# Optimization experiments

Hardware: AMD Instinct MI355X
Metric: run time of the kernel (lower is better)

The kernel has to match this reference:

```python
import jax, jax.numpy as jnp
import numpy as np

C, P, G = 80, 30000, 800       # classes, preds/class, gts/class
IOU_THR = 0.5
IMG = 1024.0                   # synthetic image size
BATCH = 16                     # images per batch (box[0] = image index)


def _make_boxes(key, n_cls, n):
    """Boxes in the module's 7-col layout: [img_idx, class, score, x1, y1, x2, y2]."""
    k1, k2, k3, k4 = jax.random.split(key, 4)
    xy = jax.random.uniform(k1, (n_cls, n, 2), minval=0.0, maxval=IMG - 128.0)
    wh = jax.random.uniform(k2, (n_cls, n, 2), minval=4.0, maxval=128.0)
    score = jax.random.uniform(k3, (n_cls, n, 1))
    img_idx = jax.random.randint(k4, (n_cls, n, 1), 0, BATCH).astype(jnp.float32)
    cls = jnp.zeros((n_cls, n, 1), jnp.float32)
    return jnp.concatenate([img_idx, cls, score, xy, xy + wh], axis=-1)


def setup_inputs() -> dict:
    key = jax.random.key(0)
    kp, kg = jax.random.split(key)
    return {"pred_boxes": _make_boxes(kp, C, P), "gt_boxes": _make_boxes(kg, C, G)}


def _pairwise_iou(a, b):
    # a: [P,4], b: [G,4] corner-format xyxy -> [P,G]
    lt = jnp.maximum(a[:, None, :2], b[None, :, :2])
    rb = jnp.minimum(a[:, None, 2:], b[None, :, 2:])
    wh = jnp.clip(rb - lt, 0.0)
    inter = wh[..., 0] * wh[..., 1]
    area_a = (a[:, 2] - a[:, 0]) * (a[:, 3] - a[:, 1])
    area_b = (b[:, 2] - b[:, 0]) * (b[:, 3] - b[:, 1])
    return inter / (area_a[:, None] + area_b[None, :] - inter + 1e-9)


def _ap_one_class(pb, gb):
    # pb: [P,7] preds, gb: [G,7] gts for one class
    n_p, n_g = pb.shape[0], gb.shape[0]
    order = jnp.argsort(-pb[:, 2])             # sort preds by score desc
    boxes = pb[order, 3:7]
    iou = _pairwise_iou(boxes, gb[:, 3:7])     # [P,G]
    best_iou = iou.max(axis=1)
    match = iou.argmax(axis=1)                 # best gt per pred
    valid = best_iou > IOU_THR
    p_idx = jnp.arange(n_p, dtype=jnp.int32)
    # first (highest-score) valid pred claiming each gt -> TP; later claims -> FP
    first = jnp.full((n_g,), n_p, jnp.int32).at[match].min(
        jnp.where(valid, p_idx, n_p))
    tp = (valid & (p_idx == first[match])).astype(jnp.float32)
    ctp = jnp.cumsum(tp)
    cfp = jnp.cumsum(1.0 - tp)
    recall = ctp / (n_g + 1e-9)
    precision = ctp / (ctp + cfp + 1e-9)
    # trapezoidal AP over the PR curve (torch.trapz(precisions, recalls))
    return jnp.sum((recall[1:] - recall[:-1]) * (precision[1:] + precision[:-1]) * 0.5)


def reference(pred_boxes, gt_boxes):
    # sequential map over classes keeps peak memory at one [P,G] IoU matrix
    aps = jax.lax.map(lambda ab: _ap_one_class(ab[0], ab[1]), (pred_boxes, gt_boxes))
    return jnp.mean(aps)
```

## Files before the change

### kernel.cpp

```cpp
#include <hip/hip_runtime.h>

#define C 80
#define P 30000
#define G 800
#define BS 256
#define NB 16
#define NC (NB * NB)
#define PPTM 8
#define TPBM (BS * PPTM)
#define HCH 8
#define CHSZ ((P + HCH - 1) / HCH)


__device__ __forceinline__ unsigned long long pack_key(float s, int p) {
    return ((unsigned long long)__float_as_uint(s) << 32) | (unsigned)(P - 1 - p);
}

__device__ __forceinline__ int cell_coord(float v) {
    return min(max((int)(v * (1.0f / 64.0f)), 0), NB - 1);
}

__device__ __forceinline__ int cell_of_center(float cxf, float cyf) {
    return cell_coord(cyf) * NB + cell_coord(cxf);
}

__global__ __launch_bounds__(BS) void gt_bin_kernel(
        const float* __restrict__ gt,
        unsigned short* __restrict__ gtCnt, unsigned short* __restrict__ gtOff,
        float4* __restrict__ gtBox, float* __restrict__ gtAbe,
        unsigned short* __restrict__ gtIdx,
        unsigned long long* __restrict__ gtKey, int* __restrict__ gHist,
        int* __restrict__ predCnt, int* __restrict__ predCur,
        unsigned int* __restrict__ doneCnt) {
    __shared__ int h[NC], cur[NC];
    __shared__ int gcell[G];
    const int c = blockIdx.x, tid = threadIdx.x;
    h[tid] = 0;
    predCnt[c * NC + tid] = 0;
    predCur[c * NC + tid] = 0;
    if (c == 0 && tid == 0) *doneCnt = 0u;
    for (int i = tid; i < G; i += BS) gtKey[c * G + i] = 0ull;
    for (int j = tid; j < 1024; j += BS) gHist[c * 1024 + j] = 0;
    __syncthreads();
    for (int i = tid; i < G; i += BS) {
        const float* r = gt + ((size_t)c * G + i) * 7;
        int cl = cell_of_center(0.5f * (r[3] + r[5]), 0.5f * (r[4] + r[6]));
        gcell[i] = cl;
        atomicAdd(&h[cl], 1);
    }
    __syncthreads();
    const int v = h[tid];
    cur[tid] = v;
    __syncthreads();
    for (int o = 1; o < NC; o <<= 1) {
        int t = (tid >= o) ? cur[tid - o] : 0;
        __syncthreads();
        cur[tid] += t;
        __syncthreads();
    }
    const int excl = cur[tid] - v;
    gtOff[c * NC + tid] = (unsigned short)excl;
    gtCnt[c * NC + tid] = (unsigned short)v;
    __syncthreads();
    cur[tid] = excl;
    __syncthreads();
    for (int i = tid; i < G; i += BS) {
        const float* r = gt + ((size_t)c * G + i) * 7;
        float x1 = r[3], y1 = r[4], x2 = r[5], y2 = r[6];
        int slot = atomicAdd(&cur[gcell[i]], 1);
        gtBox[c * G + slot] = make_float4(x1, y1, x2, y2);
        gtAbe[c * G + slot] = __fadd_rn(__fmul_rn(__fsub_rn(x2, x1), __fsub_rn(y2, y1)), 1e-9f);
        gtIdx[c * G + slot] = (unsigned short)i;
    }
}

__global__ __launch_bounds__(BS) void pprep_kernel(
        const float* __restrict__ pred, int* __restrict__ predCnt,
        unsigned char* __restrict__ cellB) {
    __shared__ int h[NC];
    const int c = blockIdx.y, tid = threadIdx.x;
    h[tid] = 0;
    __syncthreads();
    int p = blockIdx.x * BS + tid;
    if (p < P) {
        const float* r = pred + ((size_t)c * P + p) * 7;
        int cl = cell_of_center(0.5f * (r[3] + r[5]), 0.5f * (r[4] + r[6]));
        cellB[(size_t)c * P + p] = (unsigned char)cl;
        atomicAdd(&h[cl], 1);
    }
    __syncthreads();
    if (h[tid]) atomicAdd(&predCnt[c * NC + tid], h[tid]);
}

__global__ __launch_bounds__(BS) void pscatter_kernel(
        const unsigned char* __restrict__ cellB, const int* __restrict__ predCnt,
        int* __restrict__ predCur, unsigned short* __restrict__ pIdxS) {
    __shared__ int h[NC], base[NC], sc[NC];
    const int c = blockIdx.y, tid = threadIdx.x;
    h[tid] = 0;
    sc[tid] = predCnt[c * NC + tid];
    const int v = sc[tid];
    __syncthreads();
    int p = blockIdx.x * BS + tid;
    int cellv = 0, lr = 0;
    if (p < P) {
        cellv = cellB[(size_t)c * P + p];
        lr = atomicAdd(&h[cellv], 1);
    }
    __syncthreads();
    for (int o = 1; o < NC; o <<= 1) {
        int t = (tid >= o) ? sc[tid - o] : 0;
        __syncthreads();
        sc[tid] += t;
        __syncthreads();
    }
    if (h[tid]) base[tid] = (sc[tid] - v) + atomicAdd(&predCur[c * NC + tid], h[tid]);
    __syncthreads();
    if (p < P) pIdxS[(size_t)c * P + base[cellv] + lr] = (unsigned short)p;
}

__global__ __launch_bounds__(BS) void match10_kernel(
        const float* __restrict__ pred, const unsigned short* __restrict__ pIdxS,
        const unsigned short* __restrict__ gtOff, const unsigned short* __restrict__ gtCnt,
        const float4* __restrict__ gtBox, const float* __restrict__ gtAbe,
        const unsigned short* __restrict__ gtIdx,
        unsigned long long* __restrict__ gtKey) {
    __shared__ float4 sB[G];
    __shared__ float  sE[G];
    __shared__ unsigned short sG[G];
    __shared__ unsigned short sOff[NC], sCnt[NC];
    const int c = blockIdx.y, tid = threadIdx.x;
    const int s0 = blockIdx.x * TPBM;

    for (int i = tid; i < G; i += BS) {
        sB[i] = gtBox[c * G + i];
        sE[i] = gtAbe[c * G + i];
        sG[i] = gtIdx[c * G + i];
    }
    sOff[tid] = gtOff[c * NC + tid];
    sCnt[tid] = gtCnt[c * NC + tid];
    __syncthreads();

    const size_t cp = (size_t)c * P;
    #pragma unroll 1
    for (int rep = 0; rep < PPTM; ++rep) {
        const int slot = s0 + rep * BS + tid;
        if (slot < P) {
            const int p = pIdxS[cp + slot];
            const float* r = pred + (cp + p) * 7;
            float ax1 = r[3], ay1 = r[4], ax2 = r[5], ay2 = r[6];
            float A = __fmul_rn(__fsub_rn(ax2, ax1), __fsub_rn(ay2, ay1));
            const int x0 = cell_coord(ax1), x1 = cell_coord(ax2);
            const int y0 = cell_coord(ay1), y1 = cell_coord(ay2);
            float IN = 0.0f, SB = 1.0f;
            int mj = -1;
            for (int yy = y0; yy <= y1; ++yy) {
                const int rowb = yy * NB;
                const int jb = sOff[rowb + x0];
                const int je = sOff[rowb + x1] + sCnt[rowb + x1];
                #pragma unroll 2
                for (int j = jb; j < je; ++j) {
                    float4 b = sB[j];
                    float lx = fmaxf(ax1, b.x), ly = fmaxf(ay1, b.y);
                    float rx = fminf(ax2, b.z), ry = fminf(ay2, b.w);
                    float wx = fmaxf(__fsub_rn(rx, lx), 0.0f);
                    float wy = fmaxf(__fsub_rn(ry, ly), 0.0f);
                    float in = __fmul_rn(wx, wy);
                    float sb = __fadd_rn(A, sE[j]);
                    bool  up = __fmul_rn(in, SB) > __fmul_rn(IN, sb);
                    IN = up ? in : IN; SB = up ? sb : SB; mj = up ? j : mj;
                }
            }
            if (IN > 0.0f) {
                float4 b = sB[mj];
                float area = __fmul_rn(__fsub_rn(b.z, b.x), __fsub_rn(b.w, b.y));
                float dn = __fadd_rn(__fsub_rn(__fadd_rn(A, area), IN), 1e-9f);
                float iou = __fdiv_rn(IN, dn);
                if (iou > 0.5f) {
                    float sscore = r[2];
                    atomicMax(&gtKey[c * G + sG[mj]], pack_key(sscore, p));
                }
            }
        }
    }
}

__global__ __launch_bounds__(BS) void histf_kernel(
        const float* __restrict__ pred,
        const unsigned long long* __restrict__ gtKey,
        int* __restrict__ gHist, int* __restrict__ sortT) {
    __shared__ unsigned long long k[G];
    __shared__ unsigned long long sk[1024];
    __shared__ int h[1024];
    __shared__ int cnt;
    const int c = blockIdx.y, chunk = blockIdx.x, tid = threadIdx.x;

    if (tid == 0) cnt = 0;
    for (int j = tid; j < 1024; j += BS) { sk[j] = 0ull; h[j] = 0; }
    __syncthreads();
    for (int i = tid; i < G; i += BS) {
        unsigned long long key = gtKey[c * G + i];
        if (key != 0ull) k[atomicAdd(&cnt, 1)] = key;
    }
    __syncthreads();
    const int T = cnt;
    if (chunk == 0 && tid == 0) sortT[c] = T;

    for (int t = tid; t < T; t += BS) {
        unsigned long long key = k[t];
        int pos = 0;
        for (int u = 0; u < T; ++u) pos += (k[u] > key) ? 1 : 0;
        sk[pos] = key;
    }
    __syncthreads();

    const int start = chunk * CHSZ;
    const int end   = min(start + CHSZ, P);
    const float* pr = pred + (size_t)c * P * 7;
    for (int i = start + tid; i < end; i += BS) {
        unsigned long long kq =
            ((unsigned long long)__float_as_uint(pr[(size_t)i * 7 + 2]) << 32)
            | (unsigned)(P - 1 - i);
        int lo = 0;
        #pragma unroll
        for (int step = 512; step > 0; step >>= 1)
            if (sk[lo + step - 1] > kq) lo += step;
        atomicAdd(&h[lo], 1);
    }
    __syncthreads();
    for (int j = tid; j < 1024; j += BS)
        if (h[j]) atomicAdd(&gHist[c * 1024 + j], h[j]);
}

__global__ __launch_bounds__(BS) void ap2m_kernel(
        const int* __restrict__ sortT, const int* __restrict__ gHist,
        float* __restrict__ ap, unsigned int* __restrict__ doneCnt,
        float* __restrict__ out) {
    __shared__ int ha[1024];
    __shared__ int hb[1024];
    __shared__ float red[BS];
    const int c = blockIdx.x, tid = threadIdx.x;
    const int T = sortT[c];
    for (int j = tid; j < 1024; j += BS) ha[j] = gHist[c * 1024 + j];
    __syncthreads();
    int* src = ha; int* dst = hb;
    for (int o = 1; o < 1024; o <<= 1) {
        for (int j = tid; j < 1024; j += BS)
            dst[j] = src[j] + ((j >= o) ? src[j - o] : 0);
        __syncthreads();
        int* tmp = src; src = dst; dst = tmp;
    }
    float sum = 0.0f;
    for (int s = tid; s < T; s += BS) {
        int r = src[s] - 1;
        if (r >= 1) {
            float kf  = (float)(s + 1);
            float km  = (float)s;
            float ri  = __fdiv_rn(kf, 800.0f);
            float rim = __fdiv_rn(km, 800.0f);
            float pi  = __fdiv_rn(kf, (float)(r + 1));
            float pim = __fdiv_rn(km, (float)r);
            sum = __fadd_rn(sum,
                  __fmul_rn(__fmul_rn(__fsub_rn(ri, rim), __fadd_rn(pi, pim)), 0.5f));
        }
    }
    red[tid] = sum;
    __syncthreads();
    for (int s2 = BS / 2; s2 > 0; s2 >>= 1) {
        if (tid < s2) red[tid] = __fadd_rn(red[tid], red[tid + s2]);
        __syncthreads();
    }
    if (tid == 0) {
        ap[c] = red[0];
        __threadfence();
        unsigned int t = atomicAdd(doneCnt, 1u);
        if (t == C - 1) {
            __threadfence();
            float s = 0.0f;
            for (int c2 = 0; c2 < C; ++c2) s = __fadd_rn(s, ap[c2]);
            out[0] = __fdiv_rn(s, 80.0f);
        }
    }
}

extern "C" void kernel_launch(void* const* d_in, const int* in_sizes, int n_in,
                              void* d_out, int out_size, void* d_ws, size_t ws_size,
                              hipStream_t stream) {
    const float* pred = (const float*)d_in[0];
    const float* gt   = (const float*)d_in[1];
    float* out = (float*)d_out;

    char* ws = (char*)d_ws;
    int*                sortT      = (int*)               (ws + 0);
    float*              ap         = (float*)             (ws + 512);
    unsigned int*       doneCnt    = (unsigned int*)      (ws + 896);
    int*                predCnt    = (int*)               (ws + 1024);
    int*                predCur    = (int*)               (ws + 82944);
    unsigned short*     gtCnt      = (unsigned short*)    (ws + 164864);
    unsigned short*     gtOff      = (unsigned short*)    (ws + 205824);
    unsigned short*     gtIdx      = (unsigned short*)    (ws + 246784);
    float*              gtAbe      = (float*)             (ws + 374784);
    float4*             gtBox      = (float4*)            (ws + 630784);
    unsigned long long* gtKey      = (unsigned long long*)(ws + 1654784);
    int*                gHist      = (int*)               (ws + 2166784);
    unsigned char*      cellB      = (unsigned char*)     (ws + 2494464);
    unsigned short*     pIdxS      = (unsigned short*)    (ws + 4894464);

    const int P_BLK = (P + BS - 1) / BS;
    const int M_BLK = (P + TPBM - 1) / TPBM;

    gt_bin_kernel<<<C, BS, 0, stream>>>(gt, gtCnt, gtOff, gtBox, gtAbe, gtIdx,
                                        gtKey, gHist, predCnt, predCur, doneCnt);
    pprep_kernel<<<dim3(P_BLK, C), BS, 0, stream>>>(pred, predCnt, cellB);
    pscatter_kernel<<<dim3(P_BLK, C), BS, 0, stream>>>(cellB, predCnt, predCur, pIdxS);
    match10_kernel<<<dim3(M_BLK, C), BS, 0, stream>>>(pred, pIdxS, gtOff, gtCnt,
                                                      gtBox, gtAbe, gtIdx, gtKey);
    histf_kernel<<<dim3(HCH, C), BS, 0, stream>>>(pred, gtKey, gHist, sortT);
    ap2m_kernel<<<C, BS, 0, stream>>>(sortT, gHist, ap, doneCnt, out);
}
```

Measured before the change: 257.1 us.

## Remap match blocks to XCDs by class and prefetch all pred boxes upfront

The match kernel now uses a 1D grid whose block index is remapped so that all blocks of one class land on the same XCD (id&7), keeping that class's GT tables and gtKey atomics in one L2. It also loads all PPTM pred indices and their box coordinates into registers before the compute loop, so the gather latencies overlap instead of being serialised per iteration. The cost is higher register pressure from the 8x4 box array, which could lower occupancy.

```diff
diff --git a/kernel.cpp b/kernel.cpp
--- a/kernel.cpp
+++ b/kernel.cpp
@@ -8,6 +8,7 @@
 #define NC (NB * NB)
 #define PPTM 8
 #define TPBM (BS * PPTM)
+#define MPART ((P + TPBM - 1) / TPBM)
 #define HCH 8
 #define CHSZ ((P + HCH - 1) / HCH)
 
@@ -119,7 +120,7 @@
     if (p < P) pIdxS[(size_t)c * P + base[cellv] + lr] = (unsigned short)p;
 }
 
-__global__ __launch_bounds__(BS) void match10_kernel(
+__global__ __launch_bounds__(BS) void match11_kernel(
         const float* __restrict__ pred, const unsigned short* __restrict__ pIdxS,
         const unsigned short* __restrict__ gtOff, const unsigned short* __restrict__ gtCnt,
         const float4* __restrict__ gtBox, const float* __restrict__ gtAbe,
@@ -129,8 +130,13 @@
     __shared__ float  sE[G];
     __shared__ unsigned short sG[G];
     __shared__ unsigned short sOff[NC], sCnt[NC];
-    const int c = blockIdx.y, tid = threadIdx.x;
-    const int s0 = blockIdx.x * TPBM;
+    const int id  = blockIdx.x;
+    const int xcd = id & 7;
+    const int q   = id >> 3;
+    const int part = q % MPART;
+    const int c    = xcd + 8 * (q / MPART);
+    const int tid = threadIdx.x;
+    const int s0 = part * TPBM;
 
     for (int i = tid; i < G; i += BS) {
         sB[i] = gtBox[c * G + i];
@@ -142,13 +148,28 @@
     __syncthreads();
 
     const size_t cp = (size_t)c * P;
+
+    int pA[PPTM];
+    #pragma unroll
+    for (int rep = 0; rep < PPTM; ++rep) {
+        const int slot = s0 + rep * BS + tid;
+        pA[rep] = (slot < P) ? (int)pIdxS[cp + slot] : -1;
+    }
+    float bx[PPTM][4];
+    #pragma unroll
+    for (int rep = 0; rep < PPTM; ++rep) {
+        if (pA[rep] >= 0) {
+            const float* r = pred + (cp + pA[rep]) * 7;
+            bx[rep][0] = r[3]; bx[rep][1] = r[4];
+            bx[rep][2] = r[5]; bx[rep][3] = r[6];
+        }
+    }
     #pragma unroll 1
     for (int rep = 0; rep < PPTM; ++rep) {
-        const int slot = s0 + rep * BS + tid;
-        if (slot < P) {
-            const int p = pIdxS[cp + slot];
-            const float* r = pred + (cp + p) * 7;
-            float ax1 = r[3], ay1 = r[4], ax2 = r[5], ay2 = r[6];
+        if (pA[rep] >= 0) {
+            const int p = pA[rep];
+            float ax1 = bx[rep][0], ay1 = bx[rep][1];
+            float ax2 = bx[rep][2], ay2 = bx[rep][3];
             float A = __fmul_rn(__fsub_rn(ax2, ax1), __fsub_rn(ay2, ay1));
             const int x0 = cell_coord(ax1), x1 = cell_coord(ax2);
             const int y0 = cell_coord(ay1), y1 = cell_coord(ay2);
@@ -177,7 +198,7 @@
                 float dn = __fadd_rn(__fsub_rn(__fadd_rn(A, area), IN), 1e-9f);
                 float iou = __fdiv_rn(IN, dn);
                 if (iou > 0.5f) {
-                    float sscore = r[2];
+                    float sscore = pred[(cp + p) * 7 + 2];
                     atomicMax(&gtKey[c * G + sG[mj]], pack_key(sscore, p));
                 }
             }
@@ -307,14 +328,13 @@
     unsigned short*     pIdxS      = (unsigned short*)    (ws + 4894464);
 
     const int P_BLK = (P + BS - 1) / BS;
-    const int M_BLK = (P + TPBM - 1) / TPBM;
 
     gt_bin_kernel<<<C, BS, 0, stream>>>(gt, gtCnt, gtOff, gtBox, gtAbe, gtIdx,
                                         gtKey, gHist, predCnt, predCur, doneCnt);
     pprep_kernel<<<dim3(P_BLK, C), BS, 0, stream>>>(pred, predCnt, cellB);
     pscatter_kernel<<<dim3(P_BLK, C), BS, 0, stream>>>(cellB, predCnt, predCur, pIdxS);
-    match10_kernel<<<dim3(M_BLK, C), BS, 0, stream>>>(pred, pIdxS, gtOff, gtCnt,
-                                                      gtBox, gtAbe, gtIdx, gtKey);
+    match11_kernel<<<MPART * C, BS, 0, stream>>>(pred, pIdxS, gtOff, gtCnt,
+                                                 gtBox, gtAbe, gtIdx, gtKey);
     histf_kernel<<<dim3(HCH, C), BS, 0, stream>>>(pred, gtKey, gHist, sortT);
     ap2m_kernel<<<C, BS, 0, stream>>>(sortT, gHist, ap, doneCnt, out);
 }
```

New measurement: 291.0 us. +13.2%, slower.
